# Performance work log

Measured on AMD Instinct MI355X. Metric: run time of the kernel, lower is better.

Reference implementation:

```python
import jax, jax.numpy as jnp
import numpy as np

N, E = 12288, 196608
IN_DIM, HID, HEADS, EMB, K = 128, 256, 4, 16, 2
NEG_SLOPE = 0.2


def gat_layer(x, src, dst, W, a_s, a_d, b, heads, out_dim):
    # x: [N, Fin]; src/dst: [E'] (self-loops already appended)
    n = x.shape[0]
    h = (x @ W).reshape(n, heads, out_dim)                 # [N,H,F]
    alpha_src = jnp.einsum('nhf,hf->nh', h, a_s)           # [N,H]
    alpha_dst = jnp.einsum('nhf,hf->nh', h, a_d)
    e = jax.nn.leaky_relu(alpha_src[src] + alpha_dst[dst], NEG_SLOPE)  # [E,H]
    # softmax over incoming edges per destination node
    m = jax.ops.segment_max(e, dst, num_segments=n)
    ex = jnp.exp(e - m[dst])
    s = jax.ops.segment_sum(ex, dst, num_segments=n)
    alpha = ex / s[dst]                                    # [E,H]
    msg = h[src] * alpha[..., None]                        # [E,H,F]
    agg = jax.ops.segment_sum(msg, dst, num_segments=n)    # [N,H,F]
    return agg.reshape(n, heads * out_dim) + b


def setup_inputs() -> dict:
    key = jax.random.key(0)
    ks = jax.random.split(key, 16)
    x = jax.random.normal(ks[0], (N, IN_DIM), dtype=jnp.float32)
    edge_index = jax.random.randint(ks[1], (2, E), 0, N, dtype=jnp.int32)

    def glorot(k, shape):
        fan = shape[0] + shape[-1]
        return jax.random.normal(k, shape, dtype=jnp.float32) * jnp.sqrt(2.0 / fan)

    inp = {"x": x, "edge_index": edge_index}
    inp["W1"] = glorot(ks[2], (IN_DIM, HEADS * HID))
    inp["as1"] = glorot(ks[3], (HEADS, HID))
    inp["ad1"] = glorot(ks[4], (HEADS, HID))
    inp["b1"] = jnp.zeros((HEADS * HID,), jnp.float32)
    inp["W2"] = glorot(ks[5], (HEADS * HID, HEADS * HID))
    inp["as2"] = glorot(ks[6], (HEADS, HID))
    inp["ad2"] = glorot(ks[7], (HEADS, HID))
    inp["b2"] = jnp.zeros((HEADS * HID,), jnp.float32)
    # layer 3: 1024 -> 16, 1 head
    inp["W3"] = glorot(ks[8], (HEADS * HID, EMB))
    inp["as3"] = glorot(ks[9], (1, EMB))
    inp["ad3"] = glorot(ks[10], (1, EMB))
    inp["b3"] = jnp.zeros((EMB,), jnp.float32)
    inp["centers"] = jax.random.normal(ks[11], (K, EMB), dtype=jnp.float32)
    return inp


def reference(x, edge_index, W1, as1, ad1, b1, W2, as2, ad2, b2, W3, as3, ad3, b3, centers):
    n = x.shape[0]
    loop = jnp.arange(n, dtype=edge_index.dtype)
    src = jnp.concatenate([edge_index[0], loop])
    dst = jnp.concatenate([edge_index[1], loop])

    h = jax.nn.elu(gat_layer(x, src, dst, W1, as1, ad1, b1, HEADS, HID))
    h = jax.nn.elu(gat_layer(h, src, dst, W2, as2, ad2, b2, HEADS, HID))
    z = gat_layer(h, src, dst, W3, as3, ad3, b3, 1, EMB)   # [N,EMB]

    adj_recon = jax.nn.sigmoid(z @ z.T)                    # [N,N]

    # Student-t soft assignment
    d2 = jnp.sum((z[:, None, :] - centers[None, :, :]) ** 2, axis=2)  # [N,K]
    q = 1.0 / (1.0 + d2)
    q = q / jnp.sum(q, axis=1, keepdims=True)
    return z, adj_recon, q
```

## Files before the change

kernel.cpp:

```cpp
#include <hip/hip_runtime.h>
#include <hip/hip_bf16.h>
#include <math.h>

#define N_NODES 12288
#define N_EDGES 196608
#define EP_EDGES (N_EDGES + N_NODES)
#define HEADS 4
#define HID 256
#define FDIM 1024
#define EMB 16
#define NEG_SLOPE 0.2f

typedef __attribute__((ext_vector_type(8))) short short8;
typedef __attribute__((ext_vector_type(4))) float f32x4;
typedef __attribute__((ext_vector_type(2))) float f32x2;

__device__ __forceinline__ unsigned short f2bf(float f) {
  unsigned int u = __float_as_uint(f);
  u = (u + 0x7FFFu + ((u >> 16) & 1u)) >> 16;
  return (unsigned short)u;
}
__device__ __forceinline__ float bf2f(unsigned short h) {
  return __uint_as_float(((unsigned int)h) << 16);
}

__device__ __forceinline__ void t_tile_hi(const float* __restrict__ W,
                                          unsigned short* __restrict__ Th,
                                          int K, int N, int k0, int n0,
                                          int t, float (*tile)[33]) {
  int rr = t >> 3, cc = (t & 7) * 4;
  float4 v = *reinterpret_cast<const float4*>(&W[(size_t)(k0 + rr) * N + n0 + cc]);
  tile[rr][cc + 0] = v.x; tile[rr][cc + 1] = v.y; tile[rr][cc + 2] = v.z; tile[rr][cc + 3] = v.w;
  __syncthreads();
  ushort4 h;
  h.x = f2bf(tile[cc + 0][rr]);
  h.y = f2bf(tile[cc + 1][rr]);
  h.z = f2bf(tile[cc + 2][rr]);
  h.w = f2bf(tile[cc + 3][rr]);
  *reinterpret_cast<ushort4*>(&Th[(size_t)(n0 + rr) * K + k0 + cc]) = h;
}

#define HIST_BLKS (EP_EDGES / 256)
__global__ __launch_bounds__(256) void k_hist_prep(const int* __restrict__ ei,
                                                   int* __restrict__ cnt,
                                                   const float* __restrict__ x,
                                                   unsigned int* __restrict__ x8,
                                                   const float* __restrict__ W1,
                                                   unsigned short* __restrict__ w1tHi,
                                                   const float* __restrict__ W2,
                                                   unsigned short* __restrict__ w2tHi,
                                                   const float* __restrict__ as1,
                                                   const float* __restrict__ ad1,
                                                   float* __restrict__ wa,
                                                   const float* __restrict__ W3,
                                                   unsigned short* __restrict__ w3t) {
  __shared__ float tile[32][33];
  int b = blockIdx.x, t = threadIdx.x;
  if (b < HIST_BLKS) {
    int i = b * 256 + t;
    if (i < EP_EDGES) {
      int d = (i < N_EDGES) ? ei[N_EDGES + i] : (i - N_EDGES);
      atomicAdd(&cnt[d], 1);
    }
  } else if (b < HIST_BLKS + 1536) {
    int i = (b - HIST_BLKS) * 256 + t;
    float4 v = *reinterpret_cast<const float4*>(&x[(size_t)i * 4]);
    int w = __builtin_amdgcn_cvt_pk_fp8_f32(v.x, v.y, 0, false);
    w = __builtin_amdgcn_cvt_pk_fp8_f32(v.z, v.w, w, true);
    x8[i] = (unsigned int)w;
  } else if (b < HIST_BLKS + 1536 + 128) {
    int tt = b - HIST_BLKS - 1536;
    t_tile_hi(W1, w1tHi, 128, FDIM, (tt >> 5) * 32, (tt & 31) * 32, t, tile);
  } else if (b < HIST_BLKS + 1536 + 128 + 1024) {
    int tt = b - HIST_BLKS - 1536 - 128;
    t_tile_hi(W2, w2tHi, FDIM, FDIM, (tt >> 5) * 32, (tt & 31) * 32, t, tile);
  } else if (b == HIST_BLKS + 1536 + 128 + 1024) {
    for (int idx = t; idx < 1024; idx += 256) {
      int sd = idx >> 9, h = (idx >> 7) & 3, k = idx & 127;
      const float* av = sd ? ad1 : as1;
      float acc = 0.f;
      for (int f = 0; f < 256; ++f)
        acc = fmaf(W1[(size_t)k * FDIM + h * 256 + f], av[h * 256 + f], acc);
      wa[idx] = acc;
    }
  } else {
    for (int idx = t; idx < 16384; idx += 256) {
      int c = idx >> 10, k = idx & 1023;
      w3t[idx] = f2bf(W3[(size_t)k * 16 + c]);
    }
  }
}

__global__ __launch_bounds__(1024) void k_scan_alpha(const int* __restrict__ cnt,
                                                     int* __restrict__ row_ptr,
                                                     int* __restrict__ bsum,
                                                     const float* __restrict__ x,
                                                     const float* __restrict__ wa,
                                                     float* __restrict__ asrc,
                                                     float* __restrict__ adst) {
  __shared__ int sd[1024];
  int tid = threadIdx.x;
  if (blockIdx.x < 12) {
    int gid = blockIdx.x * 1024 + tid;
    int v = cnt[gid];
    sd[tid] = v;
    __syncthreads();
    for (int d = 1; d < 1024; d <<= 1) {
      int t2 = (tid >= d) ? sd[tid - d] : 0;
      __syncthreads();
      sd[tid] += t2;
      __syncthreads();
    }
    row_ptr[gid] = sd[tid] - v;
    if (tid == 1023) bsum[blockIdx.x] = sd[1023];
  } else {
    int id = (blockIdx.x - 12) * 1024 + tid;
    int n = id >> 2, h = id & 3;
    const float* wsv = wa + h * 128;
    const float* wdv = wa + 512 + h * 128;
    const float* xr = x + (size_t)n * 128;
    float accs = 0.f, accd = 0.f;
#pragma unroll
    for (int k = 0; k < 128; k += 4) {
      float4 xv = *reinterpret_cast<const float4*>(&xr[k]);
      float4 s4 = *reinterpret_cast<const float4*>(&wsv[k]);
      float4 d4 = *reinterpret_cast<const float4*>(&wdv[k]);
      accs = fmaf(xv.x, s4.x, fmaf(xv.y, s4.y, fmaf(xv.z, s4.z, fmaf(xv.w, s4.w, accs))));
      accd = fmaf(xv.x, d4.x, fmaf(xv.y, d4.y, fmaf(xv.z, d4.z, fmaf(xv.w, d4.w, accd))));
    }
    asrc[n * 4 + h] = accs;
    adst[n * 4 + h] = accd;
  }
}

__global__ void k_scan23(int* __restrict__ row_ptr, const int* __restrict__ bsum) {
  int gid = blockIdx.x * 256 + threadIdx.x;
  int blk = gid >> 10;
  int boffv = 0;
  for (int j = 0; j < blk; ++j) boffv += bsum[j];
  row_ptr[gid] += boffv;
  if (gid == 0) {
    int tot = 0;
    for (int j = 0; j < 12; ++j) tot += bsum[j];
    row_ptr[N_NODES] = tot;
  }
}

__global__ void k_scatter(const int* __restrict__ ei, const int* __restrict__ row_ptr,
                          int* __restrict__ cur, int* __restrict__ csr_src) {
  int i = blockIdx.x * 256 + threadIdx.x;
  if (i >= EP_EDGES) return;
  int s, d;
  if (i < N_EDGES) { s = ei[i]; d = ei[N_EDGES + i]; }
  else             { s = i - N_EDGES; d = s; }
  int pos = row_ptr[d] + atomicAdd(&cur[d], 1);
  csr_src[pos] = s;
}

__global__ __launch_bounds__(256) void k_aggx(const unsigned int* __restrict__ x8,
                                              const float* __restrict__ asrc,
                                              const float* __restrict__ adst,
                                              const int* __restrict__ row_ptr,
                                              const int* __restrict__ csr_src,
                                              unsigned short* __restrict__ outHi) {
  int node = (blockIdx.x * 256 + threadIdx.x) >> 6;
  int lane = threadIdx.x & 63;
  int half = lane >> 5, l = lane & 31;
  int beg = row_ptr[node], end = row_ptr[node + 1];
  float4 adn = *reinterpret_cast<const float4*>(&adst[node * 4]);
  float m0 = -INFINITY, m1 = -INFINITY, m2 = -INFINITY, m3 = -INFINITY;
  float s0 = 0.f, s1 = 0.f, s2 = 0.f, s3 = 0.f;
  float acc[16];
#pragma unroll
  for (int k = 0; k < 16; ++k) acc[k] = 0.f;
  for (int e = beg + half; e < end; e += 2) {
    int sidx = csr_src[e];
    float4 av = *reinterpret_cast<const float4*>(&asrc[sidx * 4]);
    unsigned int dw = x8[(size_t)sidx * 32 + l];
    f32x2 lo = __builtin_amdgcn_cvt_pk_f32_fp8(dw, false);
    f32x2 hi = __builtin_amdgcn_cvt_pk_f32_fp8(dw, true);
    float a, nm, sc, p;
    a = av.x + adn.x; a = a > 0.f ? a : NEG_SLOPE * a;
    nm = fmaxf(m0, a); sc = __expf(m0 - nm); p = __expf(a - nm); m0 = nm;
    s0 = s0 * sc + p;
    acc[0] = acc[0] * sc + p * lo.x; acc[1] = acc[1] * sc + p * lo.y;
    acc[2] = acc[2] * sc + p * hi.x; acc[3] = acc[3] * sc + p * hi.y;
    a = av.y + adn.y; a = a > 0.f ? a : NEG_SLOPE * a;
    nm = fmaxf(m1, a); sc = __expf(m1 - nm); p = __expf(a - nm); m1 = nm;
    s1 = s1 * sc + p;
    acc[4] = acc[4] * sc + p * lo.x; acc[5] = acc[5] * sc + p * lo.y;
    acc[6] = acc[6] * sc + p * hi.x; acc[7] = acc[7] * sc + p * hi.y;
    a = av.z + adn.z; a = a > 0.f ? a : NEG_SLOPE * a;
    nm = fmaxf(m2, a); sc = __expf(m2 - nm); p = __expf(a - nm); m2 = nm;
    s2 = s2 * sc + p;
    acc[8] = acc[8] * sc + p * lo.x; acc[9] = acc[9] * sc + p * lo.y;
    acc[10] = acc[10] * sc + p * hi.x; acc[11] = acc[11] * sc + p * hi.y;
    a = av.w + adn.w; a = a > 0.f ? a : NEG_SLOPE * a;
    nm = fmaxf(m3, a); sc = __expf(m3 - nm); p = __expf(a - nm); m3 = nm;
    s3 = s3 * sc + p;
    acc[12] = acc[12] * sc + p * lo.x; acc[13] = acc[13] * sc + p * lo.y;
    acc[14] = acc[14] * sc + p * hi.x; acc[15] = acc[15] * sc + p * hi.y;
  }
  float mm[4] = {m0, m1, m2, m3};
  float ss[4] = {s0, s1, s2, s3};
#pragma unroll
  for (int h = 0; h < 4; ++h) {
    float mo = __shfl_xor(mm[h], 32);
    float so = __shfl_xor(ss[h], 32);
    float nm = fmaxf(mm[h], mo);
    float scS = __expf(mm[h] - nm);
    float scO = __expf(mo - nm);
    ss[h] = ss[h] * scS + so * scO;
#pragma unroll
    for (int k = 0; k < 4; ++k) {
      float ao = __shfl_xor(acc[h * 4 + k], 32);
      acc[h * 4 + k] = acc[h * 4 + k] * scS + ao * scO;
    }
  }
  if (half == 0) {
    size_t base = (size_t)node * 512 + l * 4;
#pragma unroll
    for (int h = 0; h < 4; ++h) {
      float inv = 1.f / ss[h];
      ushort4 o;
      o.x = f2bf(acc[h * 4 + 0] * inv);
      o.y = f2bf(acc[h * 4 + 1] * inv);
      o.z = f2bf(acc[h * 4 + 2] * inv);
      o.w = f2bf(acc[h * 4 + 3] * inv);
      *reinterpret_cast<ushort4*>(&outHi[base + h * 128]) = o;
    }
  }
}

template <int MODE>
__global__ __launch_bounds__(256) void k_gemm(const unsigned short* __restrict__ A,
                                              const unsigned short* __restrict__ B,
                                              unsigned short* __restrict__ Out,
                                              const float* __restrict__ bias,
                                              const float* __restrict__ a_s,
                                              const float* __restrict__ a_d,
                                              float* __restrict__ asrcP,
                                              float* __restrict__ adstP,
                                              int M, int N, int K, int lda) {
  __shared__ unsigned short sA[128 * 32], sB[128 * 32];
  const int tid = threadIdx.x;
  const int lane = tid & 63, wv = tid >> 6;
  const int row0 = blockIdx.y * 128, col0 = blockIdx.x * 128;
  const int mBase = (wv >> 1) * 64, nBase = (wv & 1) * 64;
  const int lane15 = lane & 15;
  const int aoff = (MODE == 1) ? (col0 >> 8) * 128 : 0;

  f32x4 acc[4][4];
#pragma unroll
  for (int m = 0; m < 4; ++m)
#pragma unroll
    for (int n = 0; n < 4; ++n) acc[m][n] = (f32x4){0.f, 0.f, 0.f, 0.f};

  int rS[2], cS[2], dS[2];
#pragma unroll
  for (int c = 0; c < 2; ++c) {
    int p = c * 4096 + tid * 16;
    int r = p >> 6, u = (p >> 4) & 3;
    int f = (r & 3) ^ ((r >> 2) & 3);
    rS[c] = r; cS[c] = (u ^ f) * 8; dS[c] = c * 2048 + tid * 8;
  }
  const int fR = (lane & 3) ^ ((lane >> 2) & 3);
  const int uprime = (((lane >> 4) ^ fR) * 8);

  for (int k0 = 0; k0 < K; k0 += 32) {
#pragma unroll
    for (int c = 0; c < 2; ++c) {
      size_t ga = (size_t)(row0 + rS[c]) * lda + aoff + k0 + cS[c];
      size_t gb = (size_t)(col0 + rS[c]) * K + k0 + cS[c];
      __builtin_amdgcn_global_load_lds((const __attribute__((address_space(1))) void*)(A + ga),
                                       (__attribute__((address_space(3))) void*)(sA + dS[c]), 16, 0, 0);
      __builtin_amdgcn_global_load_lds((const __attribute__((address_space(1))) void*)(B + gb),
                                       (__attribute__((address_space(3))) void*)(sB + dS[c]), 16, 0, 0);
    }
    __syncthreads();

    short8 a[4], b[4];
#pragma unroll
    for (int m = 0; m < 4; ++m) {
      int ia = (mBase + m * 16 + lane15) * 32 + uprime;
      a[m] = *reinterpret_cast<const short8*>(sA + ia);
      int ib = (nBase + m * 16 + lane15) * 32 + uprime;
      b[m] = *reinterpret_cast<const short8*>(sB + ib);
    }
#pragma unroll
    for (int m = 0; m < 4; ++m)
#pragma unroll
      for (int n = 0; n < 4; ++n)
        acc[m][n] = __builtin_amdgcn_mfma_f32_16x16x32_bf16(a[m], b[n], acc[m][n], 0, 0, 0);
    __syncthreads();
  }

  const int head = col0 >> 8;
  const int q = ((col0 >> 6) & 2) | (nBase >> 6);
  float asv[4], adv[4];
  if (MODE == 0) {
#pragma unroll
    for (int n = 0; n < 4; ++n) {
      int cc = col0 + nBase + n * 16 + lane15;
      asv[n] = a_s[cc];
      adv[n] = a_d[cc];
    }
  }

#pragma unroll
  for (int m = 0; m < 4; ++m) {
    int rr = row0 + mBase + m * 16 + (lane >> 4) * 4;
#pragma unroll
    for (int j = 0; j < 4; ++j) {
      if (MODE == 1) {
#pragma unroll
        for (int n = 0; n < 4; ++n) {
          int cc = col0 + nBase + n * 16 + lane15;
          float v = acc[m][n][j] + bias[cc];
          v = v > 0.f ? v : __expf(v) - 1.f;
          Out[(size_t)(rr + j) * N + cc] = f2bf(v);
        }
      } else {
        float ps = 0.f, pd = 0.f;
#pragma unroll
        for (int n = 0; n < 4; ++n) {
          int cc = col0 + nBase + n * 16 + lane15;
          float v = acc[m][n][j];
          Out[(size_t)(rr + j) * N + cc] = f2bf(v);
          ps = fmaf(v, asv[n], ps);
          pd = fmaf(v, adv[n], pd);
        }
        ps += __shfl_xor(ps, 1); pd += __shfl_xor(pd, 1);
        ps += __shfl_xor(ps, 2); pd += __shfl_xor(pd, 2);
        ps += __shfl_xor(ps, 4); pd += __shfl_xor(pd, 4);
        ps += __shfl_xor(ps, 8); pd += __shfl_xor(pd, 8);
        if (lane15 == 0) {
          asrcP[(size_t)(rr + j) * 16 + head * 4 + q] = ps;
          adstP[(size_t)(rr + j) * 16 + head * 4 + q] = pd;
        }
      }
    }
  }
}

__global__ void k_repack8(const unsigned short* __restrict__ hbf,
                          unsigned int* __restrict__ h8,
                          const float* __restrict__ asrcP,
                          const float* __restrict__ adstP,
                          float* __restrict__ asrcR,
                          float* __restrict__ adstR) {
  int b = blockIdx.x;
  if (b < 12288) {
    int i = b * 256 + threadIdx.x;
    ushort4 v = *reinterpret_cast<const ushort4*>(&hbf[(size_t)i * 4]);
    int w = __builtin_amdgcn_cvt_pk_fp8_f32(bf2f(v.x), bf2f(v.y), 0, false);
    w = __builtin_amdgcn_cvt_pk_fp8_f32(bf2f(v.z), bf2f(v.w), w, true);
    h8[i] = (unsigned int)w;
  } else {
    int i = (b - 12288) * 256 + threadIdx.x;
    float4 sq = *reinterpret_cast<const float4*>(&asrcP[(size_t)i * 4]);
    asrcR[i] = sq.x + sq.y + sq.z + sq.w;
    float4 dq = *reinterpret_cast<const float4*>(&adstP[(size_t)i * 4]);
    adstR[i] = dq.x + dq.y + dq.z + dq.w;
  }
}

__global__ __launch_bounds__(256) void k_agg4(const unsigned int* __restrict__ h8,
                                              const float* __restrict__ asrcR,
                                              const float* __restrict__ adstR,
                                              const int* __restrict__ row_ptr,
                                              const int* __restrict__ csr_src, const float* __restrict__ bias,
                                              unsigned short* __restrict__ outHi) {
  int node = (blockIdx.x * 256 + threadIdx.x) >> 6;
  int lane = threadIdx.x & 63;
  int half = lane >> 5, l = lane & 31;
  int hd = l >> 3;
  int beg = row_ptr[node], end = row_ptr[node + 1];
  float adn = adstR[node * 4 + hd];
  float m = -INFINITY, s = 0.f;
  float acc[32];
#pragma unroll
  for (int k = 0; k < 32; ++k) acc[k] = 0.f;
  for (int e = beg + half; e < end; e += 2) {
    int sidx = csr_src[e];
    float a = asrcR[sidx * 4 + hd] + adn;
    a = a > 0.f ? a : NEG_SLOPE * a;
    float nm = fmaxf(m, a);
    float sc = __expf(m - nm);
    float p  = __expf(a - nm);
    m = nm;
    s = s * sc + p;
    const unsigned int* rp = h8 + (size_t)sidx * 256 + l * 8;
    uint4 dw0 = *reinterpret_cast<const uint4*>(rp);
    uint4 dw1 = *reinterpret_cast<const uint4*>(rp + 4);
#pragma unroll
    for (int d = 0; d < 4; ++d) {
      unsigned int w = (&dw0.x)[d];
      f32x2 lo = __builtin_amdgcn_cvt_pk_f32_fp8(w, false);
      f32x2 hi = __builtin_amdgcn_cvt_pk_f32_fp8(w, true);
      acc[d * 4 + 0] = acc[d * 4 + 0] * sc + p * lo.x;
      acc[d * 4 + 1] = acc[d * 4 + 1] * sc + p * lo.y;
      acc[d * 4 + 2] = acc[d * 4 + 2] * sc + p * hi.x;
      acc[d * 4 + 3] = acc[d * 4 + 3] * sc + p * hi.y;
    }
#pragma unroll
    for (int d = 0; d < 4; ++d) {
      unsigned int w = (&dw1.x)[d];
      f32x2 lo = __builtin_amdgcn_cvt_pk_f32_fp8(w, false);
      f32x2 hi = __builtin_amdgcn_cvt_pk_f32_fp8(w, true);
      acc[16 + d * 4 + 0] = acc[16 + d * 4 + 0] * sc + p * lo.x;
      acc[16 + d * 4 + 1] = acc[16 + d * 4 + 1] * sc + p * lo.y;
      acc[16 + d * 4 + 2] = acc[16 + d * 4 + 2] * sc + p * hi.x;
      acc[16 + d * 4 + 3] = acc[16 + d * 4 + 3] * sc + p * hi.y;
    }
  }
  float mo = __shfl_xor(m, 32);
  float so = __shfl_xor(s, 32);
  float nm = fmaxf(m, mo);
  float scS = __expf(m - nm);
  float scO = __expf(mo - nm);
  s = s * scS + so * scO;
#pragma unroll
  for (int k = 0; k < 32; ++k) {
    float ao = __shfl_xor(acc[k], 32);
    acc[k] = acc[k] * scS + ao * scO;
  }
  if (half == 0) {
    float inv = 1.f / s;
    int fo = l * 32;
#pragma unroll
    for (int d = 0; d < 8; ++d) {
      float4 bv = *reinterpret_cast<const float4*>(&bias[fo + d * 4]);
      float v0 = acc[d * 4 + 0] * inv + bv.x;
      float v1 = acc[d * 4 + 1] * inv + bv.y;
      float v2 = acc[d * 4 + 2] * inv + bv.z;
      float v3 = acc[d * 4 + 3] * inv + bv.w;
      v0 = v0 > 0.f ? v0 : __expf(v0) - 1.f;
      v1 = v1 > 0.f ? v1 : __expf(v1) - 1.f;
      v2 = v2 > 0.f ? v2 : __expf(v2) - 1.f;
      v3 = v3 > 0.f ? v3 : __expf(v3) - 1.f;
      ushort4 st;
      st.x = f2bf(v0); st.y = f2bf(v1); st.z = f2bf(v2); st.w = f2bf(v3);
      *reinterpret_cast<ushort4*>(&outHi[(size_t)node * FDIM + fo + d * 4]) = st;
    }
  }
}

__global__ __launch_bounds__(256) void k_gemm_n16(const unsigned short* __restrict__ A,
                                                  const unsigned short* __restrict__ w3t,
                                                  const float* __restrict__ a_s,
                                                  const float* __restrict__ a_d,
                                                  float* __restrict__ C,
                                                  float* __restrict__ asrc,
                                                  float* __restrict__ adst) {
  int wave = (blockIdx.x * 256 + threadIdx.x) >> 6;
  int lane = threadIdx.x & 63;
  int lane15 = lane & 15;
  int row0 = wave * 16;
  int kg = (lane >> 4) * 8;
  f32x4 acc = (f32x4){0.f, 0.f, 0.f, 0.f};
  const unsigned short* Ar = A + (size_t)(row0 + lane15) * FDIM + kg;
  const unsigned short* Br = w3t + (size_t)lane15 * FDIM + kg;
  for (int k0 = 0; k0 < FDIM; k0 += 32) {
    short8 a = *reinterpret_cast<const short8*>(Ar + k0);
    short8 b = *reinterpret_cast<const short8*>(Br + k0);
    acc = __builtin_amdgcn_mfma_f32_16x16x32_bf16(a, b, acc, 0, 0, 0);
  }
  float asv = a_s[lane15], adv = a_d[lane15];
  int rbase = row0 + (lane >> 4) * 4;
#pragma unroll
  for (int j = 0; j < 4; ++j) {
    float v = acc[j];
    C[(size_t)(rbase + j) * EMB + lane15] = v;
    float ps = v * asv, pd = v * adv;
    ps += __shfl_xor(ps, 1); pd += __shfl_xor(pd, 1);
    ps += __shfl_xor(ps, 2); pd += __shfl_xor(pd, 2);
    ps += __shfl_xor(ps, 4); pd += __shfl_xor(pd, 4);
    ps += __shfl_xor(ps, 8); pd += __shfl_xor(pd, 8);
    if (lane15 == 0) { asrc[rbase + j] = ps; adst[rbase + j] = pd; }
  }
}

__global__ __launch_bounds__(256) void k_agg1(const float* __restrict__ h3, const float* __restrict__ asrc,
                                              const float* __restrict__ adst, const int* __restrict__ row_ptr,
                                              const int* __restrict__ csr_src, const float* __restrict__ bias,
                                              const float* __restrict__ centers,
                                              float* __restrict__ z, float* __restrict__ qout,
                                              unsigned short* __restrict__ zh,
                                              unsigned short* __restrict__ zl) {
  int idx = blockIdx.x * 256 + threadIdx.x;
  int node = idx >> 4, f = idx & 15;
  if (node >= N_NODES) return;
  int beg = row_ptr[node], end = row_ptr[node + 1];
  float adn = adst[node];
  float m = -INFINITY, s = 0.f, acc = 0.f;
  for (int e = beg; e < end; ++e) {
    int sidx = csr_src[e];
    float a = asrc[sidx] + adn;
    a = a > 0.f ? a : NEG_SLOPE * a;
    float nm = fmaxf(m, a);
    float sc = __expf(m - nm);
    float p  = __expf(a - nm);
    m = nm;
    s = s * sc + p;
    acc = acc * sc + p * h3[sidx * EMB + f];
  }
  float zv = acc / s + bias[f];
  z[node * EMB + f] = zv;
  unsigned short hv = f2bf(zv);
  zh[node * EMB + f] = hv;
  zl[node * EMB + f] = f2bf(zv - bf2f(hv));
  float d0 = zv - centers[f];       d0 *= d0;
  float d1 = zv - centers[EMB + f]; d1 *= d1;
  d0 += __shfl_xor(d0, 1); d1 += __shfl_xor(d1, 1);
  d0 += __shfl_xor(d0, 2); d1 += __shfl_xor(d1, 2);
  d0 += __shfl_xor(d0, 4); d1 += __shfl_xor(d1, 4);
  d0 += __shfl_xor(d0, 8); d1 += __shfl_xor(d1, 8);
  if (f == 0) {
    float q0 = 1.f / (1.f + d0), q1 = 1.f / (1.f + d1);
    float inv = 1.f / (q0 + q1);
    qout[node * 2 + 0] = q0 * inv;
    qout[node * 2 + 1] = q1 * inv;
  }
}

__global__ __launch_bounds__(256) void k_adj(const unsigned short* __restrict__ zh,
                                             const unsigned short* __restrict__ zl,
                                             float* __restrict__ adj) {
  int tid = threadIdx.x;
  int lane = tid & 63, wv = tid >> 6;
  int r0 = blockIdx.y * 128 + wv * 32, c0 = blockIdx.x * 128;
  int l15 = lane & 15, kg = lane >> 4;
  short8 zero = (short8){0, 0, 0, 0, 0, 0, 0, 0};
  short8 ah[2], al[2];
#pragma unroll
  for (int g = 0; g < 2; ++g) {
    int row = r0 + g * 16 + l15;
    if (kg < 2) {
      ah[g] = *reinterpret_cast<const short8*>(&zh[(size_t)row * EMB + kg * 8]);
      al[g] = *reinterpret_cast<const short8*>(&zl[(size_t)row * EMB + kg * 8]);
    } else { ah[g] = zero; al[g] = zero; }
  }
  short8 bh[8], bl[8];
#pragma unroll
  for (int n = 0; n < 8; ++n) {
    int col = c0 + n * 16 + l15;
    if (kg < 2) {
      bh[n] = *reinterpret_cast<const short8*>(&zh[(size_t)col * EMB + kg * 8]);
      bl[n] = *reinterpret_cast<const short8*>(&zl[(size_t)col * EMB + kg * 8]);
    } else { bh[n] = zero; bl[n] = zero; }
  }
#pragma unroll
  for (int g = 0; g < 2; ++g) {
    int rbase = r0 + g * 16 + kg * 4;
#pragma unroll
    for (int n = 0; n < 8; ++n) {
      f32x4 acc = (f32x4){0.f, 0.f, 0.f, 0.f};
      acc = __builtin_amdgcn_mfma_f32_16x16x32_bf16(ah[g], bh[n], acc, 0, 0, 0);
      acc = __builtin_amdgcn_mfma_f32_16x16x32_bf16(ah[g], bl[n], acc, 0, 0, 0);
      acc = __builtin_amdgcn_mfma_f32_16x16x32_bf16(al[g], bh[n], acc, 0, 0, 0);
      int cc = c0 + n * 16 + l15;
#pragma unroll
      for (int j = 0; j < 4; ++j) {
        float v = 1.f / (1.f + __expf(-acc[j]));
        adj[(size_t)(rbase + j) * N_NODES + cc] = v;
      }
    }
  }
}

extern "C" void kernel_launch(void* const* d_in, const int* in_sizes, int n_in,
                              void* d_out, int out_size, void* d_ws, size_t ws_size,
                              hipStream_t stream) {
  const float* x   = (const float*)d_in[0];
  const int*   ei  = (const int*)d_in[1];
  const float* W1  = (const float*)d_in[2];
  const float* as1 = (const float*)d_in[3];
  const float* ad1 = (const float*)d_in[4];
  const float* b1  = (const float*)d_in[5];
  const float* W2  = (const float*)d_in[6];
  const float* as2 = (const float*)d_in[7];
  const float* ad2 = (const float*)d_in[8];
  const float* b2  = (const float*)d_in[9];
  const float* W3  = (const float*)d_in[10];
  const float* as3 = (const float*)d_in[11];
  const float* ad3 = (const float*)d_in[12];
  const float* b3  = (const float*)d_in[13];
  const float* centers = (const float*)d_in[14];
  float* out = (float*)d_out;

  char* ws = (char*)d_ws;
  size_t off = 0;
  auto alloc = [&](size_t bytes) { void* p = ws + off; off = (off + bytes + 255) & ~(size_t)255; return p; };
  int* cnt       = (int*)alloc((size_t)N_NODES * 4);
  int* cur       = (int*)alloc((size_t)N_NODES * 4);
  int* row_ptr   = (int*)alloc((size_t)(N_NODES + 1) * 4);
  int* bsum      = (int*)alloc(64 * 4);
  int* csr_src   = (int*)alloc((size_t)EP_EDGES * 4);
  float* asrcA   = (float*)alloc((size_t)N_NODES * HEADS * 4);
  float* adstA   = (float*)alloc((size_t)N_NODES * HEADS * 4);
  float* asrcP   = (float*)alloc((size_t)N_NODES * 16 * 4);
  float* adstP   = (float*)alloc((size_t)N_NODES * 16 * 4);
  float* asrcR   = (float*)alloc((size_t)N_NODES * 4 * 4);
  float* adstR   = (float*)alloc((size_t)N_NODES * 4 * 4);
  float* asrc3   = (float*)alloc((size_t)N_NODES * 4);
  float* adst3   = (float*)alloc((size_t)N_NODES * 4);
  float* wa      = (float*)alloc(1024 * 4);
  unsigned int*   x8     = (unsigned int*)alloc((size_t)N_NODES * 128);
  unsigned short* aggxHi = (unsigned short*)alloc((size_t)N_NODES * 512 * 2);
  unsigned short* h1bf   = (unsigned short*)alloc((size_t)N_NODES * FDIM * 2);
  unsigned short* hbf    = (unsigned short*)alloc((size_t)N_NODES * FDIM * 2);
  unsigned int*   h8     = (unsigned int*)alloc((size_t)N_NODES * FDIM);
  unsigned short* agg2Hi = (unsigned short*)alloc((size_t)N_NODES * FDIM * 2);
  unsigned short* w1tHi  = (unsigned short*)alloc((size_t)FDIM * 128 * 2);
  unsigned short* w2tHi  = (unsigned short*)alloc((size_t)FDIM * FDIM * 2);
  unsigned short* w3t    = (unsigned short*)alloc((size_t)16 * FDIM * 2);
  unsigned short* zh     = (unsigned short*)alloc((size_t)N_NODES * EMB * 2);
  unsigned short* zl     = (unsigned short*)alloc((size_t)N_NODES * EMB * 2);
  float* bufZ    = (float*)alloc((size_t)N_NODES * EMB * 4);

  hipMemsetAsync(cnt, 0, (size_t)N_NODES * 8, stream);

  k_hist_prep<<<dim3(HIST_BLKS + 1536 + 128 + 1024 + 2), dim3(256), 0, stream>>>(
      ei, cnt, x, x8, W1, w1tHi, W2, w2tHi, as1, ad1, wa, W3, w3t);

  k_scan_alpha<<<dim3(12 + 48), dim3(1024), 0, stream>>>(
      cnt, row_ptr, bsum, x, wa, asrcA, adstA);

  k_scan23<<<dim3(N_NODES / 256), dim3(256), 0, stream>>>(row_ptr, bsum);
  k_scatter<<<dim3((EP_EDGES + 255) / 256), dim3(256), 0, stream>>>(ei, row_ptr, cur, csr_src);

  k_aggx<<<dim3(N_NODES / 4), dim3(256), 0, stream>>>(x8, asrcA, adstA, row_ptr, csr_src, aggxHi);
  k_gemm<1><<<dim3(FDIM / 128, N_NODES / 128), dim3(256), 0, stream>>>(
      aggxHi, w1tHi, h1bf, b1, nullptr, nullptr, nullptr, nullptr, N_NODES, FDIM, 128, 512);

  k_gemm<0><<<dim3(FDIM / 128, N_NODES / 128), dim3(256), 0, stream>>>(
      h1bf, w2tHi, hbf, nullptr, as2, ad2, asrcP, adstP, N_NODES, FDIM, FDIM, FDIM);
  k_repack8<<<dim3(12288 + N_NODES * 4 / 256), dim3(256), 0, stream>>>(
      hbf, h8, asrcP, adstP, asrcR, adstR);
  k_agg4<<<dim3(N_NODES / 4), dim3(256), 0, stream>>>(h8, asrcR, adstR, row_ptr, csr_src, b2, agg2Hi);

  k_gemm_n16<<<dim3(N_NODES / 64), dim3(256), 0, stream>>>(
      agg2Hi, w3t, as3, ad3, bufZ, asrc3, adst3);
  float* adj = out + (size_t)N_NODES * EMB;
  float* q   = adj + (size_t)N_NODES * N_NODES;
  k_agg1<<<dim3(N_NODES * EMB / 256), dim3(256), 0, stream>>>(
      bufZ, asrc3, adst3, row_ptr, csr_src, b3, centers, out, q, zh, zl);

  k_adj<<<dim3(N_NODES / 128, N_NODES / 128), dim3(256), 0, stream>>>(zh, zl, adj);
}
```

Baseline: 374.9 us.

## Fuse layer-3 projection into layer-2 aggregation epilogue

The layer-2 aggregation kernel now applies bias and ELU, then directly multiplies the 1024-wide row by the 16-column W3 in registers with wave shuffles, producing z-pre, asrc3 and adst3 per node. This removes the 24 MB bf16 write and re-read of the aggregated layer-2 output and the separate MFMA GEMM launch. In exchange each wave does 16 scalar dot-product reductions with 80 shuffles and reads W3 from cache per node, which raises register pressure and ALU work. Both wave halves compute redundantly, and precision changes from a bf16-rounded input to fp32 values.

```diff
diff --git a/kernel.cpp b/kernel.cpp
--- a/kernel.cpp
+++ b/kernel.cpp
@@ -365,12 +365,18 @@
   }
 }
 
-__global__ __launch_bounds__(256) void k_agg4(const unsigned int* __restrict__ h8,
-                                              const float* __restrict__ asrcR,
-                                              const float* __restrict__ adstR,
-                                              const int* __restrict__ row_ptr,
-                                              const int* __restrict__ csr_src, const float* __restrict__ bias,
-                                              unsigned short* __restrict__ outHi) {
+__global__ __launch_bounds__(256) void k_agg4z(const unsigned int* __restrict__ h8,
+                                               const float* __restrict__ asrcR,
+                                               const float* __restrict__ adstR,
+                                               const int* __restrict__ row_ptr,
+                                               const int* __restrict__ csr_src,
+                                               const float* __restrict__ bias,
+                                               const unsigned short* __restrict__ w3t,
+                                               const float* __restrict__ a_s3,
+                                               const float* __restrict__ a_d3,
+                                               float* __restrict__ h3,
+                                               float* __restrict__ asrc3,
+                                               float* __restrict__ adst3) {
   int node = (blockIdx.x * 256 + threadIdx.x) >> 6;
   int lane = threadIdx.x & 63;
   int half = lane >> 5, l = lane & 31;
@@ -425,59 +431,50 @@
     float ao = __shfl_xor(acc[k], 32);
     acc[k] = acc[k] * scS + ao * scO;
   }
+  float inv = 1.f / s;
+  int fo = l * 32;
+  float val[32];
+#pragma unroll
+  for (int d = 0; d < 8; ++d) {
+    float4 bv = *reinterpret_cast<const float4*>(&bias[fo + d * 4]);
+    float v0 = acc[d * 4 + 0] * inv + bv.x;
+    float v1 = acc[d * 4 + 1] * inv + bv.y;
+    float v2 = acc[d * 4 + 2] * inv + bv.z;
+    float v3 = acc[d * 4 + 3] * inv + bv.w;
+    val[d * 4 + 0] = v0 > 0.f ? v0 : __expf(v0) - 1.f;
+    val[d * 4 + 1] = v1 > 0.f ? v1 : __expf(v1) - 1.f;
+    val[d * 4 + 2] = v2 > 0.f ? v2 : __expf(v2) - 1.f;
+    val[d * 4 + 3] = v3 > 0.f ? v3 : __expf(v3) - 1.f;
+  }
+  float zval = 0.f, ps = 0.f, pd = 0.f;
+#pragma unroll
+  for (int c = 0; c < 16; ++c) {
+    const unsigned short* wr = w3t + (size_t)c * FDIM + fo;
+    float pp = 0.f;
+#pragma unroll
+    for (int k = 0; k < 32; k += 8) {
+      short8 wv = *reinterpret_cast<const short8*>(wr + k);
+      pp = fmaf(val[k + 0], bf2f((unsigned short)wv[0]),
+           fmaf(val[k + 1], bf2f((unsigned short)wv[1]),
+           fmaf(val[k + 2], bf2f((unsigned short)wv[2]),
+           fmaf(val[k + 3], bf2f((unsigned short)wv[3]),
+           fmaf(val[k + 4], bf2f((unsigned short)wv[4]),
+           fmaf(val[k + 5], bf2f((unsigned short)wv[5]),
+           fmaf(val[k + 6], bf2f((unsigned short)wv[6]),
+           fmaf(val[k + 7], bf2f((unsigned short)wv[7]), pp))))))));
+    }
+    pp += __shfl_xor(pp, 1);
+    pp += __shfl_xor(pp, 2);
+    pp += __shfl_xor(pp, 4);
+    pp += __shfl_xor(pp, 8);
+    pp += __shfl_xor(pp, 16);
+    if (l == c) zval = pp;
+    ps = fmaf(pp, a_s3[c], ps);
+    pd = fmaf(pp, a_d3[c], pd);
+  }
   if (half == 0) {
-    float inv = 1.f / s;
-    int fo = l * 32;
-#pragma unroll
-    for (int d = 0; d < 8; ++d) {
-      float4 bv = *reinterpret_cast<const float4*>(&bias[fo + d * 4]);
-      float v0 = acc[d * 4 + 0] * inv + bv.x;
-      float v1 = acc[d * 4 + 1] * inv + bv.y;
-      float v2 = acc[d * 4 + 2] * inv + bv.z;
-      float v3 = acc[d * 4 + 3] * inv + bv.w;
-      v0 = v0 > 0.f ? v0 : __expf(v0) - 1.f;
-      v1 = v1 > 0.f ? v1 : __expf(v1) - 1.f;
-      v2 = v2 > 0.f ? v2 : __expf(v2) - 1.f;
-      v3 = v3 > 0.f ? v3 : __expf(v3) - 1.f;
-      ushort4 st;
-      st.x = f2bf(v0); st.y = f2bf(v1); st.z = f2bf(v2); st.w = f2bf(v3);
-      *reinterpret_cast<ushort4*>(&outHi[(size_t)node * FDIM + fo + d * 4]) = st;
-    }
-  }
-}
-
-__global__ __launch_bounds__(256) void k_gemm_n16(const unsigned short* __restrict__ A,
-                                                  const unsigned short* __restrict__ w3t,
-                                                  const float* __restrict__ a_s,
-                                                  const float* __restrict__ a_d,
-                                                  float* __restrict__ C,
-                                                  float* __restrict__ asrc,
-                                                  float* __restrict__ adst) {
-  int wave = (blockIdx.x * 256 + threadIdx.x) >> 6;
-  int lane = threadIdx.x & 63;
-  int lane15 = lane & 15;
-  int row0 = wave * 16;
-  int kg = (lane >> 4) * 8;
-  f32x4 acc = (f32x4){0.f, 0.f, 0.f, 0.f};
-  const unsigned short* Ar = A + (size_t)(row0 + lane15) * FDIM + kg;
-  const unsigned short* Br = w3t + (size_t)lane15 * FDIM + kg;
-  for (int k0 = 0; k0 < FDIM; k0 += 32) {
-    short8 a = *reinterpret_cast<const short8*>(Ar + k0);
-    short8 b = *reinterpret_cast<const short8*>(Br + k0);
-    acc = __builtin_amdgcn_mfma_f32_16x16x32_bf16(a, b, acc, 0, 0, 0);
-  }
-  float asv = a_s[lane15], adv = a_d[lane15];
-  int rbase = row0 + (lane >> 4) * 4;
-#pragma unroll
-  for (int j = 0; j < 4; ++j) {
-    float v = acc[j];
-    C[(size_t)(rbase + j) * EMB + lane15] = v;
-    float ps = v * asv, pd = v * adv;
-    ps += __shfl_xor(ps, 1); pd += __shfl_xor(pd, 1);
-    ps += __shfl_xor(ps, 2); pd += __shfl_xor(pd, 2);
-    ps += __shfl_xor(ps, 4); pd += __shfl_xor(pd, 4);
-    ps += __shfl_xor(ps, 8); pd += __shfl_xor(pd, 8);
-    if (lane15 == 0) { asrc[rbase + j] = ps; adst[rbase + j] = pd; }
+    if (l < 16) h3[node * EMB + l] = zval;
+    if (l == 0) { asrc3[node] = ps; adst3[node] = pd; }
   }
 }
 
@@ -611,7 +608,6 @@
   unsigned short* h1bf   = (unsigned short*)alloc((size_t)N_NODES * FDIM * 2);
   unsigned short* hbf    = (unsigned short*)alloc((size_t)N_NODES * FDIM * 2);
   unsigned int*   h8     = (unsigned int*)alloc((size_t)N_NODES * FDIM);
-  unsigned short* agg2Hi = (unsigned short*)alloc((size_t)N_NODES * FDIM * 2);
   unsigned short* w1tHi  = (unsigned short*)alloc((size_t)FDIM * 128 * 2);
   unsigned short* w2tHi  = (unsigned short*)alloc((size_t)FDIM * FDIM * 2);
   unsigned short* w3t    = (unsigned short*)alloc((size_t)16 * FDIM * 2);
@@ -638,10 +634,10 @@
       h1bf, w2tHi, hbf, nullptr, as2, ad2, asrcP, adstP, N_NODES, FDIM, FDIM, FDIM);
   k_repack8<<<dim3(12288 + N_NODES * 4 / 256), dim3(256), 0, stream>>>(
       hbf, h8, asrcP, adstP, asrcR, adstR);
-  k_agg4<<<dim3(N_NODES / 4), dim3(256), 0, stream>>>(h8, asrcR, adstR, row_ptr, csr_src, b2, agg2Hi);
-
-  k_gemm_n16<<<dim3(N_NODES / 64), dim3(256), 0, stream>>>(
-      agg2Hi, w3t, as3, ad3, bufZ, asrc3, adst3);
+
+  k_agg4z<<<dim3(N_NODES / 4), dim3(256), 0, stream>>>(
+      h8, asrcR, adstR, row_ptr, csr_src, b2, w3t, as3, ad3, bufZ, asrc3, adst3);
+
   float* adj = out + (size_t)N_NODES * EMB;
   float* q   = adj + (size_t)N_NODES * N_NODES;
   k_agg1<<<dim3(N_NODES * EMB / 256), dim3(256), 0, stream>>>(
```

Result: slower. 407.2 us (+8.6%).
